# Optimization experiments

Measured on AMD Instinct MI355X. Metric: run time of the kernel, lower is better.

## Reference

```python
import jax, jax.numpy as jnp
import numpy as np


def setup_inputs() -> dict:
    key = jax.random.key(0)
    ks = jax.random.split(key, 8)
    B, C, H, W = 16, 192, 64, 64
    dt_rank, d_state = 12, 1
    return {
        "x": jax.random.normal(ks[0], (B, C, H, W), dtype=jnp.float32),
        "conv_w": jax.random.normal(ks[1], (C, 1, 5, 5), dtype=jnp.float32) * 0.1,
        "conv_b": jax.random.normal(ks[2], (C,), dtype=jnp.float32) * 0.1,
        "x_proj_w": jax.random.normal(ks[3], (dt_rank + 2 * d_state, C), dtype=jnp.float32) * (C ** -0.5),
        "dt_w": jax.random.normal(ks[4], (C, dt_rank), dtype=jnp.float32) * (dt_rank ** -0.5),
        "dt_b": jax.random.normal(ks[5], (C,), dtype=jnp.float32) * 0.1,
        "A_logs": jnp.zeros((C, d_state), dtype=jnp.float32),  # log(arange(1,d_state+1)) with d_state=1 -> 0
        "Ds": jnp.ones((C,), dtype=jnp.float32),
    }


def reference(x, conv_w, conv_b, x_proj_w, dt_w, dt_b, A_logs, Ds):
    B, C, H, W = x.shape
    L = H * W
    dt_rank = dt_w.shape[1]
    n = A_logs.shape[1]  # d_state
    # depthwise conv2d, kernel 5, padding SAME (=d_conv//2), then SiLU
    x = jax.lax.conv_general_dilated(
        x, conv_w, window_strides=(1, 1), padding='SAME',
        feature_group_count=C, dimension_numbers=('NCHW', 'OIHW', 'NCHW'))
    x = jax.nn.silu(x + conv_b[None, :, None, None])
    xs = x.reshape(B, C, L)  # (b, d, l)
    # x_proj: (dt_rank + 2n, C) @ (b, C, l)
    x_dbl = jnp.einsum('kc,bcl->bkl', x_proj_w, xs)
    dts, Bs, Cs = jnp.split(x_dbl, [dt_rank, dt_rank + n], axis=1)
    # dt projection + softplus (delta_softplus=True with delta_bias)
    delta = jax.nn.softplus(jnp.einsum('cr,brl->bcl', dt_w, dts) + dt_b[None, :, None])  # (b,d,l)
    A = -jnp.exp(A_logs)  # (d, n)
    # selective scan returning the full state trajectory h_t (b,d,n,l):
    # h_t = exp(delta_t * A) * h_{t-1} + delta_t * B_t * u_t
    a = jnp.exp(delta[:, :, None, :] * A[None, :, :, None])        # (b,d,n,l)
    b_el = delta[:, :, None, :] * Bs[:, None, :, :] * xs[:, :, None, :]  # (b,d,n,l)

    def combine(e1, e2):
        a1, b1 = e1
        a2, b2 = e2
        return (a1 * a2, a2 * b1 + b2)

    _, h = jax.lax.associative_scan(combine, (a, b_el), axis=-1)  # h: (b,d,n,l)
    state = h.reshape(B, C * n, L)
    # y = C_t * h_t + D * u (fp32, d_state=1 broadcast)
    y = state.astype(jnp.float32) * Cs.astype(jnp.float32) + xs * Ds[:, None]
    return y.reshape(B, C, H, W)
```

## Files before the change

### kernel.cpp

```cpp
#include <hip/hip_runtime.h>
#include <hip/hip_bf16.h>
#include <cstddef>

#define BB 16
#define CC 192
#define HH 64
#define WW 64
#define LL 4096
#define DTR 12
#define KK 14

__device__ __forceinline__ float silu_f(float v) {
  return v / (1.f + __expf(-v));
}

__global__ __launch_bounds__(256) void conv_silu_kernel(
    const float* __restrict__ x, const float* __restrict__ cw,
    const float* __restrict__ cb, float* __restrict__ xs) {
  const int bc = blockIdx.x;
  const int c = bc % CC;
  const int tid = threadIdx.x;
  const int lane = tid & 63;
  const int wv = tid >> 6;
  const int oy0 = wv * 16;

  float w[25];
#pragma unroll
  for (int k = 0; k < 25; ++k) w[k] = cw[c * 25 + k];
  const float bias = cb[c];

  const float* xp = x + (size_t)bc * LL + lane;
  float* op = xs + (size_t)bc * LL + lane;

  float rv[20];
#pragma unroll
  for (int r = 0; r < 20; ++r) {
    const int gr = oy0 + r - 2;
    float v = 0.f;
    if ((unsigned)gr < 64u) v = xp[gr * 64];
    rv[r] = v;
  }

  float acc[5];
#pragma unroll
  for (int i = 0; i < 5; ++i) acc[i] = 0.f;

#pragma unroll
  for (int r = 0; r < 20; ++r) {
    float v = rv[r];
    float vm2 = __shfl_up(v, 2u, 64);
    float vm1 = __shfl_up(v, 1u, 64);
    float vp1 = __shfl_down(v, 1u, 64);
    float vp2 = __shfl_down(v, 2u, 64);
    if (lane < 2) vm2 = 0.f;
    if (lane < 1) vm1 = 0.f;
    if (lane > 62) vp1 = 0.f;
    if (lane > 61) vp2 = 0.f;
    float t[5] = {vm2, vm1, v, vp1, vp2};
#pragma unroll
    for (int ky = 0; ky < 5; ++ky) {
      if (r >= ky && (r - ky) < 16) {
        float s = acc[(r - ky) % 5];
#pragma unroll
        for (int kx = 0; kx < 5; ++kx) s += w[ky * 5 + kx] * t[kx];
        acc[(r - ky) % 5] = s;
      }
    }
    if (r >= 4) {
      const int yf = oy0 + r - 4;
      float a = acc[(r - 4) % 5] + bias;
      op[yf * 64] = silu_f(a);
      acc[(r - 4) % 5] = 0.f;
    }
  }
}

__global__ __launch_bounds__(512) void proj_kernel(
    const float* __restrict__ xs, const float* __restrict__ xpw,
    float* __restrict__ xdbl) {
  const int b = blockIdx.y;
  const int l0 = blockIdx.x * 128;
  const int tid = threadIdx.x;
  const int lane = tid & 63;
  const int g = tid >> 6;

  __shared__ float part[8][KK][132];

  float2 acc[KK];
#pragma unroll
  for (int k = 0; k < KK; ++k) acc[k] = make_float2(0.f, 0.f);

  const float* bp = xs + ((size_t)(b * CC + g * 24)) * LL + l0 + lane * 2;
#pragma unroll 4
  for (int cc = 0; cc < 24; ++cc) {
    float2 v = *(const float2*)(bp + (size_t)cc * LL);
    const int c = g * 24 + cc;
#pragma unroll
    for (int k = 0; k < KK; ++k) {
      float wv = xpw[k * CC + c];
      acc[k].x += wv * v.x;
      acc[k].y += wv * v.y;
    }
  }
#pragma unroll
  for (int k = 0; k < KK; ++k)
    *(float2*)&part[g][k][lane * 2] = acc[k];
  __syncthreads();

  for (int idx = tid; idx < KK * 128; idx += 512) {
    int k = idx >> 7, ln = idx & 127;
    float v = 0.f;
#pragma unroll
    for (int p = 0; p < 8; ++p) v += part[p][k][ln];
    xdbl[((size_t)b * KK + k) * LL + l0 + ln] = v;
  }
}

__global__ __launch_bounds__(256) void scan_kernel(
    const float* __restrict__ xs, const float* __restrict__ xdbl,
    const float* __restrict__ dtw, const float* __restrict__ dtb,
    const float* __restrict__ A_logs, const float* __restrict__ Ds,
    float* __restrict__ y) {
  const int bc = blockIdx.x;
  const int b = bc / CC;
  const int c = bc - b * CC;
  const int tid = threadIdx.x;
  const int lane = tid & 63;
  const int wv = tid >> 6;

  const float Ac = -__expf(A_logs[c]);
  const float Dc = Ds[c];
  float dw[DTR];
#pragma unroll
  for (int r = 0; r < DTR; ++r) dw[r] = dtw[c * DTR + r];
  const float db = dtb[c];

  const float* xp = xs + (size_t)bc * LL;
  const float* xb = xdbl + (size_t)b * KK * LL;
  float* yp = y + (size_t)bc * LL;

  __shared__ float segA[4];
  __shared__ float segB[4];

  float PA = 1.f;
  float hB = 0.f;
  float u[16], v[16];

#pragma unroll
  for (int ck = 0; ck < 4; ++ck) {
    const int base = wv * 1024 + ck * 256 + lane * 4;
    const float4 x4 = *(const float4*)(xp + base);
    const float4 B4 = *(const float4*)(xb + 12 * LL + base);
    const float4 C4 = *(const float4*)(xb + 13 * LL + base);
    float4 dr[DTR];
#pragma unroll
    for (int r = 0; r < DTR; ++r)
      dr[r] = *(const float4*)(xb + r * LL + base);

    float av[4], bv[4];
    float aggA = 1.f, aggB = 0.f;
#pragma unroll
    for (int q = 0; q < 4; ++q) {
      float z = db;
#pragma unroll
      for (int r = 0; r < DTR; ++r) z += dw[r] * ((&dr[r].x)[q]);
      float delta = (z > 15.f) ? z : __logf(1.f + __expf(z));
      float a = __expf(delta * Ac);
      float be = delta * ((&B4.x)[q]) * ((&x4.x)[q]);
      av[q] = a;
      bv[q] = be;
      aggA = a * aggA;
      aggB = a * aggB + be;
    }

    float incA = aggA, incB = aggB;
#pragma unroll
    for (int s = 1; s < 64; s <<= 1) {
      float pA = __shfl_up(incA, (unsigned)s, 64);
      float pB = __shfl_up(incB, (unsigned)s, 64);
      if (lane >= s) {
        incB = incA * pB + incB;
        incA = incA * pA;
      }
    }
    float eA = __shfl_up(incA, 1u, 64);
    float eB = __shfl_up(incB, 1u, 64);
    if (lane == 0) { eA = 1.f; eB = 0.f; }
    const float tA = __shfl(incA, 63, 64);
    const float tB = __shfl(incB, 63, 64);

    float h = eA * hB + eB;
    float P = PA * eA;
#pragma unroll
    for (int q = 0; q < 4; ++q) {
      h = av[q] * h + bv[q];
      P = P * av[q];
      u[ck * 4 + q] = P * ((&C4.x)[q]);
      v[ck * 4 + q] = h * ((&C4.x)[q]) + ((&x4.x)[q]) * Dc;
    }

    hB = tA * hB + tB;
    PA = PA * tA;
  }

  if (lane == 0) { segA[wv] = PA; segB[wv] = hB; }
  __syncthreads();

  float carry = 0.f;
  for (int i = 0; i < wv; ++i) carry = segA[i] * carry + segB[i];

#pragma unroll
  for (int ck = 0; ck < 4; ++ck) {
    const int base = wv * 1024 + ck * 256 + lane * 4;
    float4 o;
    o.x = u[ck * 4 + 0] * carry + v[ck * 4 + 0];
    o.y = u[ck * 4 + 1] * carry + v[ck * 4 + 1];
    o.z = u[ck * 4 + 2] * carry + v[ck * 4 + 2];
    o.w = u[ck * 4 + 3] * carry + v[ck * 4 + 3];
    *(float4*)(yp + base) = o;
  }
}

extern "C" void kernel_launch(void* const* d_in, const int* in_sizes, int n_in,
                              void* d_out, int out_size, void* d_ws,
                              size_t ws_size, hipStream_t stream) {
  const float* x        = (const float*)d_in[0];
  const float* conv_w   = (const float*)d_in[1];
  const float* conv_b   = (const float*)d_in[2];
  const float* x_proj_w = (const float*)d_in[3];
  const float* dt_w     = (const float*)d_in[4];
  const float* dt_b     = (const float*)d_in[5];
  const float* A_logs   = (const float*)d_in[6];
  const float* Ds       = (const float*)d_in[7];
  float* out = (float*)d_out;

  char* ws = (char*)d_ws;
  const size_t plane_bytes = (size_t)BB * CC * LL * sizeof(float);
  float* xs   = (float*)ws;
  float* xdbl = (float*)(ws + plane_bytes);

  conv_silu_kernel<<<dim3(BB * CC), 256, 0, stream>>>(x, conv_w, conv_b, xs);
  proj_kernel<<<dim3(LL / 128, BB), 512, 0, stream>>>(xs, x_proj_w, xdbl);
  scan_kernel<<<dim3(BB * CC), 256, 0, stream>>>(xs, xdbl, dt_w, dt_b,
                                                 A_logs, Ds, out);
}
```

Before: 166.4 us.

## Move dt projection and softplus into projection kernel, materialize delta plane

Computes the dt-rank projection and softplus in the projection kernel and writes a full per-channel delta tensor, along with separate B and C rows. The scan kernel then only loads delta, B, C and x instead of twelve dt rows plus the dot product. This removes the redundant per-channel dot product in the scan, at the cost of writing and reading an extra full-size B*C*L float plane through memory.

New measurement: 174.0 us. 1.05x slower.

```diff
diff --git a/kernel.cpp b/kernel.cpp
--- a/kernel.cpp
+++ b/kernel.cpp
@@ -75,9 +75,11 @@
   }
 }
 
-__global__ __launch_bounds__(512) void proj_kernel(
+__global__ __launch_bounds__(512) void projdt_kernel(
     const float* __restrict__ xs, const float* __restrict__ xpw,
-    float* __restrict__ xdbl) {
+    const float* __restrict__ dtw, const float* __restrict__ dtb,
+    float* __restrict__ delta, float* __restrict__ Bsp,
+    float* __restrict__ Csp) {
   const int b = blockIdx.y;
   const int l0 = blockIdx.x * 128;
   const int tid = threadIdx.x;
@@ -107,18 +109,41 @@
     *(float2*)&part[g][k][lane * 2] = acc[k];
   __syncthreads();
 
-  for (int idx = tid; idx < KK * 128; idx += 512) {
-    int k = idx >> 7, ln = idx & 127;
+  const int l = tid & 127;
+  const int cg = tid >> 7;
+  float dts[DTR];
+#pragma unroll
+  for (int r = 0; r < DTR; ++r) {
     float v = 0.f;
 #pragma unroll
-    for (int p = 0; p < 8; ++p) v += part[p][k][ln];
-    xdbl[((size_t)b * KK + k) * LL + l0 + ln] = v;
+    for (int p = 0; p < 8; ++p) v += part[p][r][l];
+    dts[r] = v;
+  }
+  if (cg == 3) {
+    float vb = 0.f, vc = 0.f;
+#pragma unroll
+    for (int p = 0; p < 8; ++p) {
+      vb += part[p][12][l];
+      vc += part[p][13][l];
+    }
+    Bsp[(size_t)b * LL + l0 + l] = vb;
+    Csp[(size_t)b * LL + l0 + l] = vc;
+  }
+
+  float* dp = delta + ((size_t)b * CC + cg * 48) * LL + l0 + l;
+  for (int i = 0; i < 48; ++i) {
+    const int c = cg * 48 + i;
+    float z = dtb[c];
+#pragma unroll
+    for (int r = 0; r < DTR; ++r) z += dtw[c * DTR + r] * dts[r];
+    float d = (z > 15.f) ? z : __logf(1.f + __expf(z));
+    dp[(size_t)i * LL] = d;
   }
 }
 
 __global__ __launch_bounds__(256) void scan_kernel(
-    const float* __restrict__ xs, const float* __restrict__ xdbl,
-    const float* __restrict__ dtw, const float* __restrict__ dtb,
+    const float* __restrict__ xs, const float* __restrict__ delta,
+    const float* __restrict__ Bsp, const float* __restrict__ Csp,
     const float* __restrict__ A_logs, const float* __restrict__ Ds,
     float* __restrict__ y) {
   const int bc = blockIdx.x;
@@ -130,13 +155,11 @@
 
   const float Ac = -__expf(A_logs[c]);
   const float Dc = Ds[c];
-  float dw[DTR];
-#pragma unroll
-  for (int r = 0; r < DTR; ++r) dw[r] = dtw[c * DTR + r];
-  const float db = dtb[c];
 
   const float* xp = xs + (size_t)bc * LL;
-  const float* xb = xdbl + (size_t)b * KK * LL;
+  const float* ddp = delta + (size_t)bc * LL;
+  const float* bpp = Bsp + (size_t)b * LL;
+  const float* cpp = Csp + (size_t)b * LL;
   float* yp = y + (size_t)bc * LL;
 
   __shared__ float segA[4];
@@ -150,23 +173,17 @@
   for (int ck = 0; ck < 4; ++ck) {
     const int base = wv * 1024 + ck * 256 + lane * 4;
     const float4 x4 = *(const float4*)(xp + base);
-    const float4 B4 = *(const float4*)(xb + 12 * LL + base);
-    const float4 C4 = *(const float4*)(xb + 13 * LL + base);
-    float4 dr[DTR];
-#pragma unroll
-    for (int r = 0; r < DTR; ++r)
-      dr[r] = *(const float4*)(xb + r * LL + base);
+    const float4 d4 = *(const float4*)(ddp + base);
+    const float4 B4 = *(const float4*)(bpp + base);
+    const float4 C4 = *(const float4*)(cpp + base);
 
     float av[4], bv[4];
     float aggA = 1.f, aggB = 0.f;
 #pragma unroll
     for (int q = 0; q < 4; ++q) {
-      float z = db;
-#pragma unroll
-      for (int r = 0; r < DTR; ++r) z += dw[r] * ((&dr[r].x)[q]);
-      float delta = (z > 15.f) ? z : __logf(1.f + __expf(z));
-      float a = __expf(delta * Ac);
-      float be = delta * ((&B4.x)[q]) * ((&x4.x)[q]);
+      const float dl = (&d4.x)[q];
+      float a = __expf(dl * Ac);
+      float be = dl * ((&B4.x)[q]) * ((&x4.x)[q]);
       av[q] = a;
       bv[q] = be;
       aggA = a * aggA;
@@ -236,11 +253,15 @@
 
   char* ws = (char*)d_ws;
   const size_t plane_bytes = (size_t)BB * CC * LL * sizeof(float);
-  float* xs   = (float*)ws;
-  float* xdbl = (float*)(ws + plane_bytes);
+  const size_t bl_bytes    = (size_t)BB * LL * sizeof(float);
+  float* xs    = (float*)ws;
+  float* delta = (float*)(ws + plane_bytes);
+  float* Bsp   = (float*)(ws + 2 * plane_bytes);
+  float* Csp   = (float*)(ws + 2 * plane_bytes + bl_bytes);
 
   conv_silu_kernel<<<dim3(BB * CC), 256, 0, stream>>>(x, conv_w, conv_b, xs);
-  proj_kernel<<<dim3(LL / 128, BB), 512, 0, stream>>>(xs, x_proj_w, xdbl);
-  scan_kernel<<<dim3(BB * CC), 256, 0, stream>>>(xs, xdbl, dt_w, dt_b,
+  projdt_kernel<<<dim3(LL / 128, BB), 512, 0, stream>>>(
+      xs, x_proj_w, dt_w, dt_b, delta, Bsp, Csp);
+  scan_kernel<<<dim3(BB * CC), 256, 0, stream>>>(xs, delta, Bsp, Csp,
                                                  A_logs, Ds, out);
 }
```

## Split projection over channel halves with atomics; restructure scan into batched wave prefix

Applied to the files above, without the earlier changes.

The projection kernel now splits the channel reduction across two grid slices along z, reducing partial sums through shared-memory atomics and then global atomics into a pre-zeroed buffer. A new zero kernel clears that buffer. The scan kernel first does a serial scan within each thread over all four chunks, then runs one interleaved wave-level prefix over the four chunk aggregates instead of four dependent shuffle scans. The aim is more parallelism and more latency hiding, at the cost of an extra launch, atomic contention, and output summed in a nondeterministic order.

New measurement: 240.0 us. 44.3% more time.

```diff
diff --git a/kernel.cpp b/kernel.cpp
--- a/kernel.cpp
+++ b/kernel.cpp
@@ -12,6 +12,10 @@
 
 __device__ __forceinline__ float silu_f(float v) {
   return v / (1.f + __expf(-v));
+}
+
+__global__ __launch_bounds__(256) void zero_kernel(float4* __restrict__ p) {
+  p[blockIdx.x * 256 + threadIdx.x] = make_float4(0.f, 0.f, 0.f, 0.f);
 }
 
 __global__ __launch_bounds__(256) void conv_silu_kernel(
@@ -80,21 +84,25 @@
     float* __restrict__ xdbl) {
   const int b = blockIdx.y;
   const int l0 = blockIdx.x * 128;
+  const int half = blockIdx.z;
   const int tid = threadIdx.x;
   const int lane = tid & 63;
   const int g = tid >> 6;
 
-  __shared__ float part[8][KK][132];
+  __shared__ float part[KK][128];
+  for (int i = tid; i < KK * 128; i += 512) ((float*)part)[i] = 0.f;
+  __syncthreads();
 
   float2 acc[KK];
 #pragma unroll
   for (int k = 0; k < KK; ++k) acc[k] = make_float2(0.f, 0.f);
 
-  const float* bp = xs + ((size_t)(b * CC + g * 24)) * LL + l0 + lane * 2;
+  const int c0 = half * 96 + g * 12;
+  const float* bp = xs + ((size_t)(b * CC + c0)) * LL + l0 + lane * 2;
 #pragma unroll 4
-  for (int cc = 0; cc < 24; ++cc) {
+  for (int cc = 0; cc < 12; ++cc) {
     float2 v = *(const float2*)(bp + (size_t)cc * LL);
-    const int c = g * 24 + cc;
+    const int c = c0 + cc;
 #pragma unroll
     for (int k = 0; k < KK; ++k) {
       float wv = xpw[k * CC + c];
@@ -103,16 +111,15 @@
     }
   }
 #pragma unroll
-  for (int k = 0; k < KK; ++k)
-    *(float2*)&part[g][k][lane * 2] = acc[k];
+  for (int k = 0; k < KK; ++k) {
+    atomicAdd(&part[k][lane * 2], acc[k].x);
+    atomicAdd(&part[k][lane * 2 + 1], acc[k].y);
+  }
   __syncthreads();
 
   for (int idx = tid; idx < KK * 128; idx += 512) {
-    int k = idx >> 7, ln = idx & 127;
-    float v = 0.f;
-#pragma unroll
-    for (int p = 0; p < 8; ++p) v += part[p][k][ln];
-    xdbl[((size_t)b * KK + k) * LL + l0 + ln] = v;
+    const int k = idx >> 7, ln = idx & 127;
+    atomicAdd(&xdbl[((size_t)b * KK + k) * LL + l0 + ln], part[k][ln]);
   }
 }
 
@@ -142,9 +149,9 @@
   __shared__ float segA[4];
   __shared__ float segB[4];
 
-  float PA = 1.f;
-  float hB = 0.f;
-  float u[16], v[16];
+  float alpha[16], beta[16];
+  float aggA[4], aggB[4];
+  float av4[4][4];
 
 #pragma unroll
   for (int ck = 0; ck < 4; ++ck) {
@@ -152,71 +159,86 @@
     const float4 x4 = *(const float4*)(xp + base);
     const float4 B4 = *(const float4*)(xb + 12 * LL + base);
     const float4 C4 = *(const float4*)(xb + 13 * LL + base);
-    float4 dr[DTR];
-#pragma unroll
-    for (int r = 0; r < DTR; ++r)
-      dr[r] = *(const float4*)(xb + r * LL + base);
-
-    float av[4], bv[4];
-    float aggA = 1.f, aggB = 0.f;
+    float z4x = db, z4y = db, z4z = db, z4w = db;
+#pragma unroll
+    for (int r = 0; r < DTR; ++r) {
+      const float4 d4 = *(const float4*)(xb + r * LL + base);
+      z4x += dw[r] * d4.x;
+      z4y += dw[r] * d4.y;
+      z4z += dw[r] * d4.z;
+      z4w += dw[r] * d4.w;
+    }
+    float zz[4] = {z4x, z4y, z4z, z4w};
+    float Pl = 1.f, hl = 0.f;
 #pragma unroll
     for (int q = 0; q < 4; ++q) {
-      float z = db;
-#pragma unroll
-      for (int r = 0; r < DTR; ++r) z += dw[r] * ((&dr[r].x)[q]);
-      float delta = (z > 15.f) ? z : __logf(1.f + __expf(z));
-      float a = __expf(delta * Ac);
-      float be = delta * ((&B4.x)[q]) * ((&x4.x)[q]);
-      av[q] = a;
-      bv[q] = be;
-      aggA = a * aggA;
-      aggB = a * aggB + be;
-    }
-
-    float incA = aggA, incB = aggB;
-#pragma unroll
-    for (int s = 1; s < 64; s <<= 1) {
-      float pA = __shfl_up(incA, (unsigned)s, 64);
-      float pB = __shfl_up(incB, (unsigned)s, 64);
-      if (lane >= s) {
-        incB = incA * pB + incB;
-        incA = incA * pA;
+      const float z = zz[q];
+      const float delta = (z > 15.f) ? z : __logf(1.f + __expf(z));
+      const float a = __expf(delta * Ac);
+      const float be = delta * ((&B4.x)[q]) * ((&x4.x)[q]);
+      hl = a * hl + be;
+      Pl = Pl * a;
+      alpha[ck * 4 + q] = Pl * ((&C4.x)[q]);
+      beta[ck * 4 + q] = hl * ((&C4.x)[q]) + ((&x4.x)[q]) * Dc;
+      (void)av4;
+    }
+    aggA[ck] = Pl;
+    aggB[ck] = hl;
+  }
+
+  float iA[4], iB[4];
+#pragma unroll
+  for (int ck = 0; ck < 4; ++ck) { iA[ck] = aggA[ck]; iB[ck] = aggB[ck]; }
+#pragma unroll
+  for (int s = 1; s < 64; s <<= 1) {
+    float pA[4], pB[4];
+#pragma unroll
+    for (int ck = 0; ck < 4; ++ck) {
+      pA[ck] = __shfl_up(iA[ck], (unsigned)s, 64);
+      pB[ck] = __shfl_up(iB[ck], (unsigned)s, 64);
+    }
+    if (lane >= s) {
+#pragma unroll
+      for (int ck = 0; ck < 4; ++ck) {
+        iB[ck] = iA[ck] * pB[ck] + iB[ck];
+        iA[ck] = iA[ck] * pA[ck];
       }
     }
-    float eA = __shfl_up(incA, 1u, 64);
-    float eB = __shfl_up(incB, 1u, 64);
-    if (lane == 0) { eA = 1.f; eB = 0.f; }
-    const float tA = __shfl(incA, 63, 64);
-    const float tB = __shfl(incB, 63, 64);
-
-    float h = eA * hB + eB;
-    float P = PA * eA;
-#pragma unroll
-    for (int q = 0; q < 4; ++q) {
-      h = av[q] * h + bv[q];
-      P = P * av[q];
-      u[ck * 4 + q] = P * ((&C4.x)[q]);
-      v[ck * 4 + q] = h * ((&C4.x)[q]) + ((&x4.x)[q]) * Dc;
-    }
-
-    hB = tA * hB + tB;
-    PA = PA * tA;
-  }
-
-  if (lane == 0) { segA[wv] = PA; segB[wv] = hB; }
+  }
+  float eA[4], eB[4], tA[4], tB[4];
+#pragma unroll
+  for (int ck = 0; ck < 4; ++ck) {
+    eA[ck] = __shfl_up(iA[ck], 1u, 64);
+    eB[ck] = __shfl_up(iB[ck], 1u, 64);
+    if (lane == 0) { eA[ck] = 1.f; eB[ck] = 0.f; }
+    tA[ck] = __shfl(iA[ck], 63, 64);
+    tB[ck] = __shfl(iB[ck], 63, 64);
+  }
+
+  float Pe[4], he[4];
+  float SP = 1.f, Sh = 0.f;
+#pragma unroll
+  for (int ck = 0; ck < 4; ++ck) {
+    Pe[ck] = SP * eA[ck];
+    he[ck] = eA[ck] * Sh + eB[ck];
+    Sh = tA[ck] * Sh + tB[ck];
+    SP = SP * tA[ck];
+  }
+
+  if (lane == 0) { segA[wv] = SP; segB[wv] = Sh; }
   __syncthreads();
-
   float carry = 0.f;
   for (int i = 0; i < wv; ++i) carry = segA[i] * carry + segB[i];
 
 #pragma unroll
   for (int ck = 0; ck < 4; ++ck) {
+    const float G = Pe[ck] * carry + he[ck];
     const int base = wv * 1024 + ck * 256 + lane * 4;
     float4 o;
-    o.x = u[ck * 4 + 0] * carry + v[ck * 4 + 0];
-    o.y = u[ck * 4 + 1] * carry + v[ck * 4 + 1];
-    o.z = u[ck * 4 + 2] * carry + v[ck * 4 + 2];
-    o.w = u[ck * 4 + 3] * carry + v[ck * 4 + 3];
+    o.x = alpha[ck * 4 + 0] * G + beta[ck * 4 + 0];
+    o.y = alpha[ck * 4 + 1] * G + beta[ck * 4 + 1];
+    o.z = alpha[ck * 4 + 2] * G + beta[ck * 4 + 2];
+    o.w = alpha[ck * 4 + 3] * G + beta[ck * 4 + 3];
     *(float4*)(yp + base) = o;
   }
 }
@@ -239,8 +261,9 @@
   float* xs   = (float*)ws;
   float* xdbl = (float*)(ws + plane_bytes);
 
+  zero_kernel<<<dim3(BB * KK * LL / 1024), 256, 0, stream>>>((float4*)xdbl);
   conv_silu_kernel<<<dim3(BB * CC), 256, 0, stream>>>(x, conv_w, conv_b, xs);
-  proj_kernel<<<dim3(LL / 128, BB), 512, 0, stream>>>(xs, x_proj_w, xdbl);
+  proj_kernel<<<dim3(LL / 128, BB, 2), 512, 0, stream>>>(xs, x_proj_w, xdbl);
   scan_kernel<<<dim3(BB * CC), 256, 0, stream>>>(xs, xdbl, dt_w, dt_b,
                                                  A_logs, Ds, out);
 }
```
